# Optimization experiments

Hardware: AMD Instinct MI355X
Metric: run time of the kernel (lower is better)

Reference implementation:

```python
import jax, jax.numpy as jnp
import numpy as np

N_NODES = 100000
N_EDGES = 1600000
DIMS = [256, 128, 64, 1]  # decoder_dim=256, decoder_l=3 -> 256->128->64->1


def setup_inputs() -> dict:
    key = jax.random.key(0)
    ks = jax.random.split(key, 10)
    inp = {
        "b_z": jax.random.normal(ks[0], (N_NODES, DIMS[0]), jnp.float32),
        "src": jax.random.randint(ks[1], (N_EDGES,), 0, N_NODES, dtype=jnp.int64) if jax.config.jax_enable_x64 else jax.random.randint(ks[1], (N_EDGES,), 0, N_NODES),
        "dst": jax.random.randint(ks[2], (N_EDGES,), 0, N_NODES),
        "b_edge_weight": jax.random.uniform(ks[3], (N_EDGES,), jnp.float32),
        "b_size": 1000,
    }
    for i in range(3):
        inp[f"W{i+1}"] = jax.random.normal(ks[4 + i], (DIMS[i], DIMS[i + 1]), jnp.float32) / np.sqrt(DIMS[i]).astype(np.float32)
        inp[f"b{i+1}"] = jnp.zeros((DIMS[i + 1],), jnp.float32)
    return inp


def _gcn_layer(z, src, dst, ew, W, b, act):
    """DGL GraphConv, norm='both', weight=True, bias=True, in_feats > out_feats."""
    N = z.shape[0]
    ones = jnp.ones(src.shape[0], dtype=z.dtype)
    # unweighted structural degrees, clamped to >= 1 (DGL behavior)
    deg_out = jnp.clip(jax.ops.segment_sum(ones, src, num_segments=N), 1.0)
    deg_in = jnp.clip(jax.ops.segment_sum(ones, dst, num_segments=N), 1.0)
    norm_src = deg_out ** -0.5
    norm_dst = deg_in ** -0.5
    # src-normalize, then project (in > out so weight applied before aggregation)
    h = (z * norm_src[:, None]) @ W          # [N, out]
    m = h[src] * ew[:, None]                 # gather + edge weighting: [E, out]
    rst = jax.ops.segment_sum(m, dst, num_segments=N)  # scatter-sum to dst
    rst = rst * norm_dst[:, None] + b
    return act(rst) if act is not None else rst


def reference(b_z, src, dst, b_edge_weight, b_size, W1, b1, W2, b2, W3, b3):
    z = _gcn_layer(b_z, src, dst, b_edge_weight, W1, b1, jax.nn.relu)
    z = _gcn_layer(z, src, dst, b_edge_weight, W2, b2, jax.nn.relu)
    z = _gcn_layer(z, src, dst, b_edge_weight, W3, b3, None)  # last layer: no activation
    # nonlin_layers is empty (decoder_nonlin_out=None)
    return z.reshape(b_size, -1)
```

## Files before the change

kernel.cpp:

```cpp
#include <hip/hip_runtime.h>


constexpr int D0 = 256, D1 = 128, D2 = 64;
constexpr int NB = 1024;
constexpr int BSH = 7;
constexpr int EBLK = 4096;

typedef __attribute__((ext_vector_type(2))) float f32x2;
typedef __attribute__((ext_vector_type(4))) float f32x4;
typedef __attribute__((ext_vector_type(8))) short short8;

__device__ inline unsigned short f2bf(float f) {
  unsigned u = __builtin_bit_cast(unsigned, f);
  u += 0x7fffu + ((u >> 16) & 1u);
  return (unsigned short)(u >> 16);
}
__device__ inline float bf2f(unsigned short h) {
  unsigned u = ((unsigned)h) << 16;
  return __builtin_bit_cast(float, u);
}
__device__ inline int rdlane_i(int v, int l) { return __builtin_amdgcn_readlane(v, l); }
__device__ inline float rdlane_f(float v, int l) {
  return __builtin_bit_cast(float, __builtin_amdgcn_readlane(__builtin_bit_cast(int, v), l));
}

__global__ void k_chist2(const int* __restrict__ src, const int* __restrict__ dst,
                         int* __restrict__ bc_s, int* __restrict__ bc_d, int E) {
  __shared__ int hs[NB], hd[NB];
  for (int i = threadIdx.x; i < NB; i += 256) { hs[i] = 0; hd[i] = 0; }
  __syncthreads();
  int e0 = blockIdx.x * EBLK, e1 = min(e0 + EBLK, E);
  for (int i = e0 + threadIdx.x; i < e1; i += 256) {
    atomicAdd(&hs[src[i] >> BSH], 1);
    atomicAdd(&hd[dst[i] >> BSH], 1);
  }
  __syncthreads();
  for (int i = threadIdx.x; i < NB; i += 256) {
    bc_s[blockIdx.x * NB + i] = hs[i];
    bc_d[blockIdx.x * NB + i] = hd[i];
  }
}

__global__ void k_binscan(int* __restrict__ bc_s, int* __restrict__ bt_s,
                          int* __restrict__ bc_d, int* __restrict__ bt_d, int nbk) {
  __shared__ int part[16][17];
  int* bc = blockIdx.y ? bc_d : bc_s;
  int* bt = blockIdx.y ? bt_d : bt_s;
  const int j = threadIdx.x & 15;
  const int c = threadIdx.x >> 4;
  const int bin = blockIdx.x * 16 + j;
  const int chunk = (nbk + 15) / 16;
  const int r0 = c * chunk, r1 = min(r0 + chunk, nbk);
  int s = 0;
  for (int b = r0; b < r1; ++b) s += bc[b * NB + bin];
  part[c][j] = s;
  __syncthreads();
  int pre = 0;
  for (int q = 0; q < c; ++q) pre += part[q][j];
  int run = pre;
  for (int b = r0; b < r1; ++b) {
    int v = bc[b * NB + bin];
    bc[b * NB + bin] = run;
    run += v;
  }
  if (c == 15) bt[bin] = run;
}

__global__ void k_btscan(const int* __restrict__ bt_s, int* __restrict__ cbase_s,
                         const int* __restrict__ bt_d, int* __restrict__ cbase_d,
                         int* __restrict__ offs_end, int E) {
  __shared__ int wsum[16];
  const int* bt = blockIdx.x ? bt_d : bt_s;
  int* cbase = blockIdx.x ? cbase_d : cbase_s;
  int tid = threadIdx.x, lane = tid & 63, wid = tid >> 6;
  int v = bt[tid];
  int x = v;
#pragma unroll
  for (int d = 1; d < 64; d <<= 1) { int t = __shfl_up(x, d); if (lane >= d) x += t; }
  if (lane == 63) wsum[wid] = x;
  __syncthreads();
  if (wid == 0 && lane < 16) {
    int s = wsum[lane];
#pragma unroll
    for (int d = 1; d < 16; d <<= 1) { int t = __shfl_up(s, d, 16); if (lane >= d) s += t; }
    wsum[lane] = s;
  }
  __syncthreads();
  int excl = x - v + (wid ? wsum[wid - 1] : 0);
  cbase[tid] = excl;
  if (tid == NB - 1) cbase[NB] = E;
  if (blockIdx.x == 1 && tid == 0) *offs_end = E;
}

__global__ void k_cpart2(const int* __restrict__ src, const int* __restrict__ dst,
                         const float* __restrict__ ew,
                         const int* __restrict__ bc_s, const int* __restrict__ cbase_s,
                         const int* __restrict__ bc_d, const int* __restrict__ cbase_d,
                         int* __restrict__ recs_s, int2* __restrict__ recs_d, int E) {
  __shared__ int cs[NB], cd[NB];
  for (int i = threadIdx.x; i < NB; i += 256) {
    cs[i] = cbase_s[i] + bc_s[blockIdx.x * NB + i];
    cd[i] = cbase_d[i] + bc_d[blockIdx.x * NB + i];
  }
  __syncthreads();
  int e0 = blockIdx.x * EBLK, e1 = min(e0 + EBLK, E);
  for (int i = e0 + threadIdx.x; i < e1; i += 256) {
    int s = src[i], d = dst[i];
    int ps = atomicAdd(&cs[s >> BSH], 1);
    recs_s[ps] = s;
    int pd = atomicAdd(&cd[d >> BSH], 1);
    recs_d[pd] = int2{s | ((d & 127) << 17), __builtin_bit_cast(int, ew[i])};
  }
}

__global__ void k_finecomb(const int2* __restrict__ recs_d, const int* __restrict__ cbase_d,
                           const int* __restrict__ recs_s, const int* __restrict__ cbase_s,
                           int2* __restrict__ esw, int* __restrict__ offs,
                           float* __restrict__ nd, float* __restrict__ ns, int N) {
  __shared__ int h[128], cur[128];
  __shared__ int w0tot;
  int bin = blockIdx.x;
  int r0 = cbase_d[bin], r1 = cbase_d[bin + 1];
  int t = threadIdx.x;
  if (t < 128) h[t] = 0;
  __syncthreads();
  for (int i = r0 + t; i < r1; i += 256) atomicAdd(&h[recs_d[i].x >> 17], 1);
  __syncthreads();
  int v = 0, x = 0;
  if (t < 128) {
    v = h[t];
    x = v;
#pragma unroll
    for (int d = 1; d < 64; d <<= 1) { int tt = __shfl_up(x, d); if ((t & 63) >= d) x += tt; }
    if (t == 63) w0tot = x;
  }
  __syncthreads();
  if (t < 128) {
    int excl = x - v + (t >= 64 ? w0tot : 0);
    int node = bin * 128 + t;
    if (node < N) {
      offs[node] = r0 + excl;
      int d = v < 1 ? 1 : v;
      nd[node] = (float)(1.0 / sqrt((double)d));
    }
    cur[t] = r0 + excl;
  }
  __syncthreads();
  for (int i = r0 + t; i < r1; i += 256) {
    int2 rc = recs_d[i];
    int p = atomicAdd(&cur[rc.x >> 17], 1);
    esw[p] = int2{rc.x & 0x1ffff, rc.y};
  }
  __syncthreads();
  if (t < 128) h[t] = 0;
  __syncthreads();
  int s0 = cbase_s[bin], s1 = cbase_s[bin + 1];
  for (int i = s0 + t; i < s1; i += 256) atomicAdd(&h[recs_s[i] & 127], 1);
  __syncthreads();
  if (t < 128) {
    int node = bin * 128 + t;
    if (node < N) {
      int d = h[t] < 1 ? 1 : h[t];
      ns[node] = (float)(1.0 / sqrt((double)d));
    }
  }
}

__global__ void k_wsplit2(const float* __restrict__ W1, short* __restrict__ w1h,
                          short* __restrict__ w1l, const float* __restrict__ W2,
                          short* __restrict__ w2h, short* __restrict__ w2l) {
  int t = blockIdx.x * blockDim.x + threadIdx.x;
  if (t < D0 * D1) {
    int k = t / D1, n = t % D1;
    float f = W1[t];
    unsigned short h = f2bf(f);
    w1h[(size_t)n * D0 + k] = (short)h;
    w1l[(size_t)n * D0 + k] = (short)f2bf(f - bf2f(h));
  } else if (t < D0 * D1 + D1 * D2) {
    int i = t - D0 * D1;
    int k = i / D2, n = i % D2;
    float f = W2[i];
    unsigned short h = f2bf(f);
    w2h[(size_t)n * D1 + k] = (short)h;
    w2l[(size_t)n * D1 + k] = (short)f2bf(f - bf2f(h));
  }
}

template <int K, int N, int WR, int WC>
__launch_bounds__(256, 2)
__global__ void k_gemm_mfma(const float* __restrict__ A, const float* __restrict__ ns,
                            const short* __restrict__ Wth, const short* __restrict__ Wtl,
                            float* __restrict__ C, int M) {
  constexpr int MR = 128 / WR / 16;
  constexpr int NC = N / WC / 16;
  __shared__ short8 Ah[4 * 128], Al[4 * 128];
  __shared__ short8 Bh[4 * N], Bl[4 * N];
  const int t = threadIdx.x;
  const int block_row = blockIdx.x * 128;
  const int lane = t & 63, wid = t >> 6;
  const int wr = wid / WC, wc = wid % WC;
  const int rowbase = wr * (128 / WR), colbase = wc * (N / WC);
  const int c = lane >> 4, lr = lane & 15;
  f32x4 acc[MR][NC] = {};
  const int r = t & 127;
  const int grow = block_row + r;
  float nsv = 0.f;
  if (t < 128 && grow < M) nsv = ns[grow];

  for (int k0 = 0; k0 < K; k0 += 32) {
    if (t < 128) {
      f32x4 v[8];
      if (grow < M) {
        const f32x4* ap = (const f32x4*)(A + (size_t)grow * K + k0);
#pragma unroll
        for (int i = 0; i < 8; ++i) v[i] = ap[i] * nsv;
      } else {
#pragma unroll
        for (int i = 0; i < 8; ++i) v[i] = f32x4{0.f, 0.f, 0.f, 0.f};
      }
#pragma unroll
      for (int cc = 0; cc < 4; ++cc) {
        short8 hi, lo;
#pragma unroll
        for (int i = 0; i < 8; ++i) {
          float f = v[cc * 2 + (i >> 2)][i & 3];
          unsigned short h = f2bf(f);
          hi[i] = (short)h;
          lo[i] = (short)f2bf(f - bf2f(h));
        }
        Ah[cc * 128 + r] = hi;
        Al[cc * 128 + r] = lo;
      }
    } else {
      const int tt = t - 128;
#pragma unroll
      for (int id = tt; id < N * 4; id += 128) {
        int col = id & (N - 1);
        int cb = id / N;
        Bh[cb * N + col] = *(const short8*)(Wth + (size_t)col * K + k0 + cb * 8);
        Bl[cb * N + col] = *(const short8*)(Wtl + (size_t)col * K + k0 + cb * 8);
      }
    }
    __syncthreads();
    short8 ah[MR], al[MR], bh[NC], bl[NC];
#pragma unroll
    for (int m = 0; m < MR; ++m) {
      int row = rowbase + m * 16 + lr;
      ah[m] = Ah[c * 128 + row];
      al[m] = Al[c * 128 + row];
    }
#pragma unroll
    for (int n = 0; n < NC; ++n) {
      int col = colbase + n * 16 + lr;
      bh[n] = Bh[c * N + col];
      bl[n] = Bl[c * N + col];
    }
#pragma unroll
    for (int m = 0; m < MR; ++m)
#pragma unroll
      for (int n = 0; n < NC; ++n) {
        acc[m][n] = __builtin_amdgcn_mfma_f32_16x16x32_bf16(ah[m], bh[n], acc[m][n], 0, 0, 0);
        acc[m][n] = __builtin_amdgcn_mfma_f32_16x16x32_bf16(ah[m], bl[n], acc[m][n], 0, 0, 0);
        acc[m][n] = __builtin_amdgcn_mfma_f32_16x16x32_bf16(al[m], bh[n], acc[m][n], 0, 0, 0);
      }
    __syncthreads();
  }
#pragma unroll
  for (int m = 0; m < MR; ++m) {
#pragma unroll
    for (int j = 0; j < 4; ++j) {
      int row = block_row + rowbase + m * 16 + (lane >> 4) * 4 + j;
      if (row < M) {
#pragma unroll
        for (int n = 0; n < NC; ++n)
          C[(size_t)row * N + colbase + n * 16 + lr] = acc[m][n][j];
      }
    }
  }
}

__launch_bounds__(256, 4)
__global__ void k_agg128f(const float* __restrict__ h, const int* __restrict__ offs,
                          const int2* __restrict__ esw, const float* __restrict__ nd,
                          const float* __restrict__ b1v, const float* __restrict__ ns,
                          const short* __restrict__ w2h, const short* __restrict__ w2l,
                          float* __restrict__ h2, int M) {
  __shared__ unsigned Ah32[16 * 64], Al32[16 * 64];
  const int t = threadIdx.x, lane = t & 63, wid = t >> 6;
  const int base = blockIdx.x * 16;
  const int nb0 = base + wid * 4;
  const f32x4* hp4 = (const f32x4*)h;
  const int p = lane & 31;
  const int hi = lane >> 5;
  f32x4 bv = ((const f32x4*)b1v)[p];
  int ov = offs[min(nb0 + min(lane, 5), M)];
  int S0[4], S1[4];
#pragma unroll
  for (int q = 0; q < 4; ++q) { S0[q] = rdlane_i(ov, q); S1[q] = rdlane_i(ov, q + 1); }
  int2 ecur{0, 0};
  { int kk = S0[0] + lane; if (kk < S1[0]) ecur = esw[kk]; }
#pragma unroll
  for (int q = 0; q < 4; ++q) {
    const int row = wid * 4 + q;
    const int node = nb0 + q;
    int2 enxt{0, 0};
    if (q < 3) { int kk = S0[q + 1] + lane; if (kk < S1[q + 1]) enxt = esw[kk]; }
    unsigned hw0 = 0, hw1 = 0, lw0 = 0, lw1 = 0;
    if (node < M) {
      const int s0 = S0[q], s1 = S1[q];
      f32x4 acc = {};
      int2 e = ecur;
      for (int bb = s0; bb < s1; bb += 64) {
        if (bb != s0) { int kk = bb + lane; e = (kk < s1) ? esw[kk] : int2{0, 0}; }
        int sidx = e.x;
        float wt = __builtin_bit_cast(float, e.y);
        int cnt = min(64, s1 - bb);
        for (int jj = 0; jj < cnt; jj += 16) {
          f32x4 v[8];
#pragma unroll
          for (int u = 0; u < 8; ++u) {
            int r0 = rdlane_i(sidx, jj + 2 * u);
            int r1 = rdlane_i(sidx, jj + 2 * u + 1);
            int s = hi ? r1 : r0;
            v[u] = hp4[(size_t)(unsigned)s * 32 + p];
          }
          __builtin_amdgcn_sched_barrier(0);
#pragma unroll
          for (int u = 0; u < 8; ++u) {
            float w0 = rdlane_f(wt, jj + 2 * u);
            float w1 = rdlane_f(wt, jj + 2 * u + 1);
            float wu = hi ? w1 : w0;
            acc[0] += v[u][0] * wu;
            acc[1] += v[u][1] * wu;
            acc[2] += v[u][2] * wu;
            acc[3] += v[u][3] * wu;
          }
        }
      }
      f32x4 o;
#pragma unroll
      for (int i = 0; i < 4; ++i) o[i] = acc[i] + __shfl_xor(acc[i], 32);
      float ndv = nd[node], nsv = ns[node];
      float z[4];
#pragma unroll
      for (int i = 0; i < 4; ++i) z[i] = fmaxf(o[i] * ndv + bv[i], 0.f) * nsv;
      unsigned short h0 = f2bf(z[0]), h1b = f2bf(z[1]), h2b = f2bf(z[2]), h3b = f2bf(z[3]);
      hw0 = (unsigned)h0 | ((unsigned)h1b << 16);
      hw1 = (unsigned)h2b | ((unsigned)h3b << 16);
      lw0 = (unsigned)f2bf(z[0] - bf2f(h0)) | ((unsigned)f2bf(z[1] - bf2f(h1b)) << 16);
      lw1 = (unsigned)f2bf(z[2] - bf2f(h2b)) | ((unsigned)f2bf(z[3] - bf2f(h3b)) << 16);
    }
    if (lane < 32) {
      int widx = (2 * p) ^ ((row & 7) << 2);
      *(uint2*)&Ah32[row * 64 + widx] = uint2{hw0, hw1};
      *(uint2*)&Al32[row * 64 + widx] = uint2{lw0, lw1};
    }
    ecur = enxt;
  }
  __syncthreads();
  const int colB = wid * 16 + (lane & 15);
  const int koff = (lane >> 4) * 8;
  short8 bh[4], bl[4];
#pragma unroll
  for (int ks = 0; ks < 4; ++ks) {
    bh[ks] = *(const short8*)(w2h + (size_t)colB * 128 + ks * 32 + koff);
    bl[ks] = *(const short8*)(w2l + (size_t)colB * 128 + ks * 32 + koff);
  }
  const int arow = lane & 15, ac = lane >> 4;
  f32x4 acc = {};
#pragma unroll
  for (int ks = 0; ks < 4; ++ks) {
    int bidx = arow * 64 + ((ks * 16 + ac * 4) ^ ((arow & 7) << 2));
    short8 ah = *(const short8*)(Ah32 + bidx);
    short8 al = *(const short8*)(Al32 + bidx);
    acc = __builtin_amdgcn_mfma_f32_16x16x32_bf16(ah, bh[ks], acc, 0, 0, 0);
    acc = __builtin_amdgcn_mfma_f32_16x16x32_bf16(ah, bl[ks], acc, 0, 0, 0);
    acc = __builtin_amdgcn_mfma_f32_16x16x32_bf16(al, bh[ks], acc, 0, 0, 0);
  }
  const int crow = (lane >> 4) * 4;
  const int col = wid * 16 + (lane & 15);
#pragma unroll
  for (int j = 0; j < 4; ++j) {
    int node = base + crow + j;
    if (node < M) h2[(size_t)node * 64 + col] = acc[j];
  }
}

__global__ void k_agg64mv(const float* __restrict__ h, const int* __restrict__ offs,
                          const int2* __restrict__ esw, const float* __restrict__ nd,
                          const float* __restrict__ b2, const float* __restrict__ W3,
                          const float* __restrict__ ns, float* __restrict__ h3, int M) {
  const int lane = threadIdx.x & 63;
  const int wave = blockIdx.x * (blockDim.x >> 6) + (threadIdx.x >> 6);
  const int nb0 = wave * 4;
  if (nb0 >= M) return;
  const f32x4* hp4 = (const f32x4*)h;
  const int p = lane & 15;
  const int q4 = lane >> 4;
  const bool qb0 = q4 & 1, qb1 = q4 & 2;
  f32x4 bv = ((const f32x4*)b2)[p];
  f32x4 w3v = ((const f32x4*)W3)[p];
  int ov = offs[min(nb0 + min(lane, 5), M)];
  int S0[4], S1[4];
#pragma unroll
  for (int q = 0; q < 4; ++q) { S0[q] = rdlane_i(ov, q); S1[q] = rdlane_i(ov, q + 1); }
  int2 ecur{0, 0};
  { int kk = S0[0] + lane; if (kk < S1[0]) ecur = esw[kk]; }
#pragma unroll
  for (int q = 0; q < 4; ++q) {
    const int node = nb0 + q;
    int2 enxt{0, 0};
    if (q < 3) { int kk = S0[q + 1] + lane; if (kk < S1[q + 1]) enxt = esw[kk]; }
    if (node < M) {
      const int s0 = S0[q], s1 = S1[q];
      f32x4 acc = {};
      int2 e = ecur;
      for (int bb = s0; bb < s1; bb += 64) {
        if (bb != s0) { int kk = bb + lane; e = (kk < s1) ? esw[kk] : int2{0, 0}; }
        int sidx = e.x;
        float wt = __builtin_bit_cast(float, e.y);
        int cnt = min(64, s1 - bb);
        for (int jj = 0; jj < cnt; jj += 32) {
          f32x4 v[8];
#pragma unroll
          for (int u = 0; u < 8; ++u) {
            int ei = jj + 4 * u;
            int r0 = rdlane_i(sidx, ei), r1 = rdlane_i(sidx, ei + 1);
            int r2 = rdlane_i(sidx, ei + 2), r3 = rdlane_i(sidx, ei + 3);
            int c01 = qb0 ? r1 : r0;
            int c23 = qb0 ? r3 : r2;
            int s = qb1 ? c23 : c01;
            v[u] = hp4[(size_t)(unsigned)s * 16 + p];
          }
          __builtin_amdgcn_sched_barrier(0);
#pragma unroll
          for (int u = 0; u < 8; ++u) {
            int ei = jj + 4 * u;
            float w0 = rdlane_f(wt, ei), w1 = rdlane_f(wt, ei + 1);
            float w2 = rdlane_f(wt, ei + 2), w3s = rdlane_f(wt, ei + 3);
            float c01 = qb0 ? w1 : w0;
            float c23 = qb0 ? w3s : w2;
            float wu = qb1 ? c23 : c01;
            acc[0] += v[u][0] * wu;
            acc[1] += v[u][1] * wu;
            acc[2] += v[u][2] * wu;
            acc[3] += v[u][3] * wu;
          }
        }
      }
#pragma unroll
      for (int i = 0; i < 4; ++i) {
        acc[i] += __shfl_xor(acc[i], 16);
        acc[i] += __shfl_xor(acc[i], 32);
      }
      float ndv = nd[node];
      float dp = 0.f;
#pragma unroll
      for (int i = 0; i < 4; ++i) dp += fmaxf(acc[i] * ndv + bv[i], 0.f) * w3v[i];
#pragma unroll
      for (int d = 8; d; d >>= 1) dp += __shfl_xor(dp, d);
      if (lane == 0) h3[node] = dp * ns[node];
    }
    ecur = enxt;
  }
}

__global__ void k_aggfin(const float* __restrict__ h3, const int* __restrict__ offs,
                         const int2* __restrict__ esw, const float* __restrict__ nd,
                         const float* __restrict__ b3, float* __restrict__ out, int M) {
  int i = blockIdx.x * blockDim.x + threadIdx.x;
  if (i >= M) return;
  int s0 = offs[i], s1 = offs[i + 1];
  float acc = 0.f;
  int k = s0;
  for (; k + 4 <= s1; k += 4) {
    int2 e0 = esw[k], e1 = esw[k + 1], e2 = esw[k + 2], e3 = esw[k + 3];
    acc += h3[e0.x] * __builtin_bit_cast(float, e0.y)
         + h3[e1.x] * __builtin_bit_cast(float, e1.y)
         + h3[e2.x] * __builtin_bit_cast(float, e2.y)
         + h3[e3.x] * __builtin_bit_cast(float, e3.y);
  }
  for (; k < s1; ++k) {
    int2 e = esw[k];
    acc += h3[e.x] * __builtin_bit_cast(float, e.y);
  }
  out[i] = acc * nd[i] + b3[0];
}

extern "C" void kernel_launch(void* const* d_in, const int* in_sizes, int n_in,
                              void* d_out, int out_size, void* d_ws, size_t ws_size,
                              hipStream_t stream) {
  const float* b_z = (const float*)d_in[0];
  const int*   src = (const int*)d_in[1];
  const int*   dst = (const int*)d_in[2];
  const float* ew  = (const float*)d_in[3];
  const float* W1  = (const float*)d_in[5];
  const float* b1  = (const float*)d_in[6];
  const float* W2  = (const float*)d_in[7];
  const float* b2  = (const float*)d_in[8];
  const float* W3  = (const float*)d_in[9];
  const float* b3  = (const float*)d_in[10];
  const int N = in_sizes[0] / D0;
  const int E = in_sizes[1];
  float* out = (float*)d_out;

  char* ws = (char*)d_ws;
  size_t off_b = 0;
  auto alloc = [&](size_t bytes) -> void* {
    void* p = ws + off_b;
    off_b += (bytes + 255) & ~(size_t)255;
    return p;
  };
  const int nbk = (E + EBLK - 1) / EBLK;
  int*   bc_s    = (int*)alloc((size_t)nbk * NB * 4);
  int*   bc_d    = (int*)alloc((size_t)nbk * NB * 4);
  int*   bt_s    = (int*)alloc((size_t)NB * 4);
  int*   bt_d    = (int*)alloc((size_t)NB * 4);
  int*   cbase_s = (int*)alloc((size_t)(NB + 1) * 4);
  int*   cbase_d = (int*)alloc((size_t)(NB + 1) * 4);
  int*   offs    = (int*)alloc((size_t)(N + 1) * 4);
  int2*  esw     = (int2*)alloc((size_t)E * 8);
  float* nsrc    = (float*)alloc((size_t)N * 4);
  float* ndst    = (float*)alloc((size_t)N * 4);
  float* h1      = (float*)alloc((size_t)N * D1 * 4);
  float* h2      = (float*)alloc((size_t)N * D2 * 4);
  float* h3      = (float*)alloc((size_t)N * 4);
  short* wt1h    = (short*)alloc((size_t)D0 * D1 * 2);
  short* wt1l    = (short*)alloc((size_t)D0 * D1 * 2);
  short* wt2h    = (short*)alloc((size_t)D1 * D2 * 2);
  short* wt2l    = (short*)alloc((size_t)D1 * D2 * 2);
  int2*  recs_d = (int2*)h1;
  int*   recs_s = (int*)((char*)h1 + ((size_t)16 << 20));

  k_chist2<<<nbk, 256, 0, stream>>>(src, dst, bc_s, bc_d, E);
  k_binscan<<<dim3(NB / 16, 2), 256, 0, stream>>>(bc_s, bt_s, bc_d, bt_d, nbk);
  k_btscan<<<2, 1024, 0, stream>>>(bt_s, cbase_s, bt_d, cbase_d, &offs[N], E);
  k_cpart2<<<nbk, 256, 0, stream>>>(src, dst, ew, bc_s, cbase_s, bc_d, cbase_d,
                                    recs_s, recs_d, E);
  k_finecomb<<<NB, 256, 0, stream>>>(recs_d, cbase_d, recs_s, cbase_s, esw, offs,
                                     ndst, nsrc, N);
  k_wsplit2<<<(D0 * D1 + D1 * D2 + 255) / 256, 256, 0, stream>>>(W1, wt1h, wt1l,
                                                                 W2, wt2h, wt2l);

  k_gemm_mfma<D0, D1, 2, 2><<<(N + 127) / 128, 256, 0, stream>>>(b_z, nsrc, wt1h, wt1l, h1, N);
  k_agg128f<<<(N + 15) / 16, 256, 0, stream>>>(h1, offs, esw, ndst, b1, nsrc,
                                               wt2h, wt2l, h2, N);
  k_agg64mv<<<(N + 15) / 16, 256, 0, stream>>>(h2, offs, esw, ndst, b2, W3, nsrc, h3, N);
  k_aggfin<<<(N + 255) / 256, 256, 0, stream>>>(h3, offs, esw, ndst, b3, out, N);
}
```

Measured before the change: 323.8 us.

## Split layer-1 aggregation into feature-sliced gather kernel plus separate MFMA GEMM

Replaces the fused aggregate-then-GEMM kernel for layer 1 with a gather kernel that splits the 128 features into four 32-wide slices across interleaved blocks, writes the ReLU output to a new fp32 buffer, and then runs the existing MFMA GEMM template for the 128->64 projection. Slicing is meant to shrink the working set of each gather pass for better cache locality, at the cost of an extra full fp32 intermediate round-trip and re-reading edge lists four times. It also reduces EBLK for the CSR build, rewrites the final scalar aggregation with 16-wide batched loads, and relocates the recs_s scratch into the new buffer.

```diff
diff --git a/kernel.cpp b/kernel.cpp
--- a/kernel.cpp
+++ b/kernel.cpp
@@ -4,7 +4,7 @@
 constexpr int D0 = 256, D1 = 128, D2 = 64;
 constexpr int NB = 1024;
 constexpr int BSH = 7;
-constexpr int EBLK = 4096;
+constexpr int EBLK = 1024;
 
 typedef __attribute__((ext_vector_type(2))) float f32x2;
 typedef __attribute__((ext_vector_type(4))) float f32x4;
@@ -279,20 +279,17 @@
   }
 }
 
-__launch_bounds__(256, 4)
-__global__ void k_agg128f(const float* __restrict__ h, const int* __restrict__ offs,
+__global__ void k_agg128s(const float* __restrict__ h1, const int* __restrict__ offs,
                           const int2* __restrict__ esw, const float* __restrict__ nd,
-                          const float* __restrict__ b1v, const float* __restrict__ ns,
-                          const short* __restrict__ w2h, const short* __restrict__ w2l,
-                          float* __restrict__ h2, int M) {
-  __shared__ unsigned Ah32[16 * 64], Al32[16 * 64];
-  const int t = threadIdx.x, lane = t & 63, wid = t >> 6;
-  const int base = blockIdx.x * 16;
-  const int nb0 = base + wid * 4;
-  const f32x4* hp4 = (const f32x4*)h;
-  const int p = lane & 31;
-  const int hi = lane >> 5;
-  f32x4 bv = ((const f32x4*)b1v)[p];
+                          const float* __restrict__ b1, float* __restrict__ z1, int M) {
+  const int lane = threadIdx.x & 63, wid = threadIdx.x >> 6;
+  const int bid = blockIdx.x;
+  const int sl = (bid & 7) >> 1;
+  const int ng = ((bid >> 3) << 1) | (bid & 1);
+  const int nb0 = ng * 16 + wid * 4;
+  const int p = lane & 31, hi = lane >> 5;
+  const int feat = sl * 32 + p;
+  float bv = b1[feat];
   int ov = offs[min(nb0 + min(lane, 5), M)];
   int S0[4], S1[4];
 #pragma unroll
@@ -301,14 +298,12 @@
   { int kk = S0[0] + lane; if (kk < S1[0]) ecur = esw[kk]; }
 #pragma unroll
   for (int q = 0; q < 4; ++q) {
-    const int row = wid * 4 + q;
     const int node = nb0 + q;
     int2 enxt{0, 0};
     if (q < 3) { int kk = S0[q + 1] + lane; if (kk < S1[q + 1]) enxt = esw[kk]; }
-    unsigned hw0 = 0, hw1 = 0, lw0 = 0, lw1 = 0;
     if (node < M) {
       const int s0 = S0[q], s1 = S1[q];
-      f32x4 acc = {};
+      float acc = 0.f;
       int2 e = ecur;
       for (int bb = s0; bb < s1; bb += 64) {
         if (bb != s0) { int kk = bb + lane; e = (kk < s1) ? esw[kk] : int2{0, 0}; }
@@ -316,73 +311,30 @@
         float wt = __builtin_bit_cast(float, e.y);
         int cnt = min(64, s1 - bb);
         for (int jj = 0; jj < cnt; jj += 16) {
-          f32x4 v[8];
+          float v[8];
 #pragma unroll
           for (int u = 0; u < 8; ++u) {
             int r0 = rdlane_i(sidx, jj + 2 * u);
             int r1 = rdlane_i(sidx, jj + 2 * u + 1);
             int s = hi ? r1 : r0;
-            v[u] = hp4[(size_t)(unsigned)s * 32 + p];
+            v[u] = h1[(size_t)(unsigned)s * 128 + feat];
           }
           __builtin_amdgcn_sched_barrier(0);
 #pragma unroll
           for (int u = 0; u < 8; ++u) {
             float w0 = rdlane_f(wt, jj + 2 * u);
             float w1 = rdlane_f(wt, jj + 2 * u + 1);
-            float wu = hi ? w1 : w0;
-            acc[0] += v[u][0] * wu;
-            acc[1] += v[u][1] * wu;
-            acc[2] += v[u][2] * wu;
-            acc[3] += v[u][3] * wu;
+            acc += v[u] * (hi ? w1 : w0);
           }
         }
       }
-      f32x4 o;
-#pragma unroll
-      for (int i = 0; i < 4; ++i) o[i] = acc[i] + __shfl_xor(acc[i], 32);
-      float ndv = nd[node], nsv = ns[node];
-      float z[4];
-#pragma unroll
-      for (int i = 0; i < 4; ++i) z[i] = fmaxf(o[i] * ndv + bv[i], 0.f) * nsv;
-      unsigned short h0 = f2bf(z[0]), h1b = f2bf(z[1]), h2b = f2bf(z[2]), h3b = f2bf(z[3]);
-      hw0 = (unsigned)h0 | ((unsigned)h1b << 16);
-      hw1 = (unsigned)h2b | ((unsigned)h3b << 16);
-      lw0 = (unsigned)f2bf(z[0] - bf2f(h0)) | ((unsigned)f2bf(z[1] - bf2f(h1b)) << 16);
-      lw1 = (unsigned)f2bf(z[2] - bf2f(h2b)) | ((unsigned)f2bf(z[3] - bf2f(h3b)) << 16);
-    }
-    if (lane < 32) {
-      int widx = (2 * p) ^ ((row & 7) << 2);
-      *(uint2*)&Ah32[row * 64 + widx] = uint2{hw0, hw1};
-      *(uint2*)&Al32[row * 64 + widx] = uint2{lw0, lw1};
+      acc += __shfl_xor(acc, 32);
+      if (hi == 0) {
+        float z = fmaxf(acc * nd[node] + bv, 0.f);
+        z1[(size_t)node * 128 + feat] = z;
+      }
     }
     ecur = enxt;
-  }
-  __syncthreads();
-  const int colB = wid * 16 + (lane & 15);
-  const int koff = (lane >> 4) * 8;
-  short8 bh[4], bl[4];
-#pragma unroll
-  for (int ks = 0; ks < 4; ++ks) {
-    bh[ks] = *(const short8*)(w2h + (size_t)colB * 128 + ks * 32 + koff);
-    bl[ks] = *(const short8*)(w2l + (size_t)colB * 128 + ks * 32 + koff);
-  }
-  const int arow = lane & 15, ac = lane >> 4;
-  f32x4 acc = {};
-#pragma unroll
-  for (int ks = 0; ks < 4; ++ks) {
-    int bidx = arow * 64 + ((ks * 16 + ac * 4) ^ ((arow & 7) << 2));
-    short8 ah = *(const short8*)(Ah32 + bidx);
-    short8 al = *(const short8*)(Al32 + bidx);
-    acc = __builtin_amdgcn_mfma_f32_16x16x32_bf16(ah, bh[ks], acc, 0, 0, 0);
-    acc = __builtin_amdgcn_mfma_f32_16x16x32_bf16(ah, bl[ks], acc, 0, 0, 0);
-    acc = __builtin_amdgcn_mfma_f32_16x16x32_bf16(al, bh[ks], acc, 0, 0, 0);
-  }
-  const int crow = (lane >> 4) * 4;
-  const int col = wid * 16 + (lane & 15);
-#pragma unroll
-  for (int j = 0; j < 4; ++j) {
-    int node = base + crow + j;
-    if (node < M) h2[(size_t)node * 64 + col] = acc[j];
   }
 }
 
@@ -465,6 +417,7 @@
   }
 }
 
+__launch_bounds__(256)
 __global__ void k_aggfin(const float* __restrict__ h3, const int* __restrict__ offs,
                          const int2* __restrict__ esw, const float* __restrict__ nd,
                          const float* __restrict__ b3, float* __restrict__ out, int M) {
@@ -472,17 +425,18 @@
   if (i >= M) return;
   int s0 = offs[i], s1 = offs[i + 1];
   float acc = 0.f;
-  int k = s0;
-  for (; k + 4 <= s1; k += 4) {
-    int2 e0 = esw[k], e1 = esw[k + 1], e2 = esw[k + 2], e3 = esw[k + 3];
-    acc += h3[e0.x] * __builtin_bit_cast(float, e0.y)
-         + h3[e1.x] * __builtin_bit_cast(float, e1.y)
-         + h3[e2.x] * __builtin_bit_cast(float, e2.y)
-         + h3[e3.x] * __builtin_bit_cast(float, e3.y);
-  }
-  for (; k < s1; ++k) {
-    int2 e = esw[k];
-    acc += h3[e.x] * __builtin_bit_cast(float, e.y);
+  for (int k0 = s0; k0 < s1; k0 += 16) {
+    int nn = min(16, s1 - k0);
+    int2 e[16];
+    float hv[16];
+#pragma unroll
+    for (int u = 0; u < 16; ++u) e[u] = esw[k0 + min(u, nn - 1)];
+#pragma unroll
+    for (int u = 0; u < 16; ++u) hv[u] = h3[e[u].x];
+    __builtin_amdgcn_sched_barrier(0);
+#pragma unroll
+    for (int u = 0; u < 16; ++u)
+      if (u < nn) acc += hv[u] * __builtin_bit_cast(float, e[u].y);
   }
   out[i] = acc * nd[i] + b3[0];
 }
@@ -523,6 +477,7 @@
   float* nsrc    = (float*)alloc((size_t)N * 4);
   float* ndst    = (float*)alloc((size_t)N * 4);
   float* h1      = (float*)alloc((size_t)N * D1 * 4);
+  float* z1      = (float*)alloc((size_t)N * D1 * 4);
   float* h2      = (float*)alloc((size_t)N * D2 * 4);
   float* h3      = (float*)alloc((size_t)N * 4);
   short* wt1h    = (short*)alloc((size_t)D0 * D1 * 2);
@@ -530,7 +485,7 @@
   short* wt2h    = (short*)alloc((size_t)D1 * D2 * 2);
   short* wt2l    = (short*)alloc((size_t)D1 * D2 * 2);
   int2*  recs_d = (int2*)h1;
-  int*   recs_s = (int*)((char*)h1 + ((size_t)16 << 20));
+  int*   recs_s = (int*)z1;
 
   k_chist2<<<nbk, 256, 0, stream>>>(src, dst, bc_s, bc_d, E);
   k_binscan<<<dim3(NB / 16, 2), 256, 0, stream>>>(bc_s, bt_s, bc_d, bt_d, nbk);
@@ -543,8 +498,10 @@
                                                                  W2, wt2h, wt2l);
 
   k_gemm_mfma<D0, D1, 2, 2><<<(N + 127) / 128, 256, 0, stream>>>(b_z, nsrc, wt1h, wt1l, h1, N);
-  k_agg128f<<<(N + 15) / 16, 256, 0, stream>>>(h1, offs, esw, ndst, b1, nsrc,
-                                               wt2h, wt2l, h2, N);
+  int NG = (N + 15) / 16;
+  if (NG & 1) ++NG;
+  k_agg128s<<<NG * 4, 256, 0, stream>>>(h1, offs, esw, ndst, b1, z1, N);
+  k_gemm_mfma<D1, D2, 4, 1><<<(N + 127) / 128, 256, 0, stream>>>(z1, nsrc, wt2h, wt2l, h2, N);
   k_agg64mv<<<(N + 15) / 16, 256, 0, stream>>>(h2, offs, esw, ndst, b2, W3, nsrc, h3, N);
   k_aggfin<<<(N + 255) / 256, 256, 0, stream>>>(h3, offs, esw, ndst, b3, out, N);
 }
```

New measurement: 436.4 us. 1.35x slower.

## Stage edge metadata in LDS for gathers and batch final aggregation loads

Applied to the files above, without the earlier changes.

In the 128- and 64-wide aggregation kernels, each wave now writes its 64 edge (src, weight) pairs to a per-wave LDS buffer, and lanes read their own edges from LDS. This replaces the long chains of readlane and select instructions used to broadcast indices and weights. The final scalar aggregation now loads 16 edges and their h3 values at once before accumulating, exposing more memory-level parallelism. The histogram edge block size is halved to launch more blocks. These add LDS traffic and rely on wave-synchronous LDS visibility without an explicit barrier.

```diff
diff --git a/kernel.cpp b/kernel.cpp
--- a/kernel.cpp
+++ b/kernel.cpp
@@ -4,7 +4,7 @@
 constexpr int D0 = 256, D1 = 128, D2 = 64;
 constexpr int NB = 1024;
 constexpr int BSH = 7;
-constexpr int EBLK = 4096;
+constexpr int EBLK = 2048;
 
 typedef __attribute__((ext_vector_type(2))) float f32x2;
 typedef __attribute__((ext_vector_type(4))) float f32x4;
@@ -20,9 +20,6 @@
   return __builtin_bit_cast(float, u);
 }
 __device__ inline int rdlane_i(int v, int l) { return __builtin_amdgcn_readlane(v, l); }
-__device__ inline float rdlane_f(float v, int l) {
-  return __builtin_bit_cast(float, __builtin_amdgcn_readlane(__builtin_bit_cast(int, v), l));
-}
 
 __global__ void k_chist2(const int* __restrict__ src, const int* __restrict__ dst,
                          int* __restrict__ bc_s, int* __restrict__ bc_d, int E) {
@@ -286,6 +283,7 @@
                           const short* __restrict__ w2h, const short* __restrict__ w2l,
                           float* __restrict__ h2, int M) {
   __shared__ unsigned Ah32[16 * 64], Al32[16 * 64];
+  __shared__ int2 emeta[4][64];
   const int t = threadIdx.x, lane = t & 63, wid = t >> 6;
   const int base = blockIdx.x * 16;
   const int nb0 = base + wid * 4;
@@ -312,24 +310,20 @@
       int2 e = ecur;
       for (int bb = s0; bb < s1; bb += 64) {
         if (bb != s0) { int kk = bb + lane; e = (kk < s1) ? esw[kk] : int2{0, 0}; }
-        int sidx = e.x;
-        float wt = __builtin_bit_cast(float, e.y);
+        emeta[wid][lane] = e;
         int cnt = min(64, s1 - bb);
         for (int jj = 0; jj < cnt; jj += 16) {
+          int2 em[8];
           f32x4 v[8];
 #pragma unroll
+          for (int u = 0; u < 8; ++u) em[u] = emeta[wid][jj + 2 * u + hi];
+#pragma unroll
+          for (int u = 0; u < 8; ++u)
+            v[u] = hp4[(size_t)(unsigned)em[u].x * 32 + p];
+          __builtin_amdgcn_sched_barrier(0);
+#pragma unroll
           for (int u = 0; u < 8; ++u) {
-            int r0 = rdlane_i(sidx, jj + 2 * u);
-            int r1 = rdlane_i(sidx, jj + 2 * u + 1);
-            int s = hi ? r1 : r0;
-            v[u] = hp4[(size_t)(unsigned)s * 32 + p];
-          }
-          __builtin_amdgcn_sched_barrier(0);
-#pragma unroll
-          for (int u = 0; u < 8; ++u) {
-            float w0 = rdlane_f(wt, jj + 2 * u);
-            float w1 = rdlane_f(wt, jj + 2 * u + 1);
-            float wu = hi ? w1 : w0;
+            float wu = __builtin_bit_cast(float, em[u].y);
             acc[0] += v[u][0] * wu;
             acc[1] += v[u][1] * wu;
             acc[2] += v[u][2] * wu;
@@ -390,14 +384,14 @@
                           const int2* __restrict__ esw, const float* __restrict__ nd,
                           const float* __restrict__ b2, const float* __restrict__ W3,
                           const float* __restrict__ ns, float* __restrict__ h3, int M) {
-  const int lane = threadIdx.x & 63;
-  const int wave = blockIdx.x * (blockDim.x >> 6) + (threadIdx.x >> 6);
+  __shared__ int2 emeta[4][64];
+  const int lane = threadIdx.x & 63, wid = threadIdx.x >> 6;
+  const int wave = blockIdx.x * (blockDim.x >> 6) + wid;
   const int nb0 = wave * 4;
   if (nb0 >= M) return;
   const f32x4* hp4 = (const f32x4*)h;
   const int p = lane & 15;
   const int q4 = lane >> 4;
-  const bool qb0 = q4 & 1, qb1 = q4 & 2;
   f32x4 bv = ((const f32x4*)b2)[p];
   f32x4 w3v = ((const f32x4*)W3)[p];
   int ov = offs[min(nb0 + min(lane, 5), M)];
@@ -417,30 +411,20 @@
       int2 e = ecur;
       for (int bb = s0; bb < s1; bb += 64) {
         if (bb != s0) { int kk = bb + lane; e = (kk < s1) ? esw[kk] : int2{0, 0}; }
-        int sidx = e.x;
-        float wt = __builtin_bit_cast(float, e.y);
+        emeta[wid][lane] = e;
         int cnt = min(64, s1 - bb);
         for (int jj = 0; jj < cnt; jj += 32) {
+          int2 em[8];
           f32x4 v[8];
 #pragma unroll
+          for (int u = 0; u < 8; ++u) em[u] = emeta[wid][jj + 4 * u + q4];
+#pragma unroll
+          for (int u = 0; u < 8; ++u)
+            v[u] = hp4[(size_t)(unsigned)em[u].x * 16 + p];
+          __builtin_amdgcn_sched_barrier(0);
+#pragma unroll
           for (int u = 0; u < 8; ++u) {
-            int ei = jj + 4 * u;
-            int r0 = rdlane_i(sidx, ei), r1 = rdlane_i(sidx, ei + 1);
-            int r2 = rdlane_i(sidx, ei + 2), r3 = rdlane_i(sidx, ei + 3);
-            int c01 = qb0 ? r1 : r0;
-            int c23 = qb0 ? r3 : r2;
-            int s = qb1 ? c23 : c01;
-            v[u] = hp4[(size_t)(unsigned)s * 16 + p];
-          }
-          __builtin_amdgcn_sched_barrier(0);
-#pragma unroll
-          for (int u = 0; u < 8; ++u) {
-            int ei = jj + 4 * u;
-            float w0 = rdlane_f(wt, ei), w1 = rdlane_f(wt, ei + 1);
-            float w2 = rdlane_f(wt, ei + 2), w3s = rdlane_f(wt, ei + 3);
-            float c01 = qb0 ? w1 : w0;
-            float c23 = qb0 ? w3s : w2;
-            float wu = qb1 ? c23 : c01;
+            float wu = __builtin_bit_cast(float, em[u].y);
             acc[0] += v[u][0] * wu;
             acc[1] += v[u][1] * wu;
             acc[2] += v[u][2] * wu;
@@ -465,6 +449,7 @@
   }
 }
 
+__launch_bounds__(256)
 __global__ void k_aggfin(const float* __restrict__ h3, const int* __restrict__ offs,
                          const int2* __restrict__ esw, const float* __restrict__ nd,
                          const float* __restrict__ b3, float* __restrict__ out, int M) {
@@ -472,17 +457,18 @@
   if (i >= M) return;
   int s0 = offs[i], s1 = offs[i + 1];
   float acc = 0.f;
-  int k = s0;
-  for (; k + 4 <= s1; k += 4) {
-    int2 e0 = esw[k], e1 = esw[k + 1], e2 = esw[k + 2], e3 = esw[k + 3];
-    acc += h3[e0.x] * __builtin_bit_cast(float, e0.y)
-         + h3[e1.x] * __builtin_bit_cast(float, e1.y)
-         + h3[e2.x] * __builtin_bit_cast(float, e2.y)
-         + h3[e3.x] * __builtin_bit_cast(float, e3.y);
-  }
-  for (; k < s1; ++k) {
-    int2 e = esw[k];
-    acc += h3[e.x] * __builtin_bit_cast(float, e.y);
+  for (int k0 = s0; k0 < s1; k0 += 16) {
+    int nn = min(16, s1 - k0);
+    int2 e[16];
+    float hv[16];
+#pragma unroll
+    for (int u = 0; u < 16; ++u) e[u] = esw[k0 + min(u, nn - 1)];
+#pragma unroll
+    for (int u = 0; u < 16; ++u) hv[u] = h3[e[u].x];
+    __builtin_amdgcn_sched_barrier(0);
+#pragma unroll
+    for (int u = 0; u < 16; ++u)
+      if (u < nn) acc += hv[u] * __builtin_bit_cast(float, e[u].y);
   }
   out[i] = acc * nd[i] + b3[0];
 }
```

Measured after the change: 334.1 us. 3.2% more time.
